# Kernel tuning notes

Measured on AMD Instinct MI355X. Metric: run time of the kernel, lower is better.

The kernel has to match this reference:

```python
import jax, jax.numpy as jnp
import numpy as np

N = 20000   # nodes
E = 160000  # edges
C = 512     # input_size / channels
D = 16      # edge_size
H = 256     # hidden_size
EPS = 1e-5  # BatchNorm eps (eval mode, init running stats: mean=0, var=1)


def setup_inputs() -> dict:
    key = jax.random.key(0)
    ks = jax.random.split(key, 24)
    w = lambda k, shape: (jax.random.normal(k, shape, jnp.float32) * 0.02)
    inp = {
        "x": jax.random.normal(ks[0], (N, C), jnp.float32),
        "edge_index": jax.random.randint(ks[1], (2, E), 0, N, jnp.int32),
        "edge_attr": jax.random.normal(ks[2], (E, D), jnp.float32),
        "goal_feat": jax.random.normal(ks[3], (N, C), jnp.float32),
        # CGConv 1
        "Wf1": w(ks[4], (2 * C + D, C)), "bf1": jnp.zeros((C,), jnp.float32),
        "Ws1": w(ks[5], (2 * C + D, C)), "bs1": jnp.zeros((C,), jnp.float32),
        "g1": jnp.ones((C,), jnp.float32), "be1": jnp.zeros((C,), jnp.float32),
        # CGConv 2
        "Wf2": w(ks[6], (2 * C + D, C)), "bf2": jnp.zeros((C,), jnp.float32),
        "Ws2": w(ks[7], (2 * C + D, C)), "bs2": jnp.zeros((C,), jnp.float32),
        "g2": jnp.ones((C,), jnp.float32), "be2": jnp.zeros((C,), jnp.float32),
        # GCNConv 3, 4
        "W3": w(ks[8], (C, H)), "b3": jnp.zeros((H,), jnp.float32),
        "W4": w(ks[9], (H, H)), "b4": jnp.zeros((H,), jnp.float32),
        # distance MLP: Lin(H+C -> C), ReLU, Lin(C -> 1)
        "Wd1": w(ks[10], (H + C, C)), "bd1": jnp.zeros((C,), jnp.float32),
        "Wd2": w(ks[11], (C, 1)), "bd2": jnp.zeros((1,), jnp.float32),
    }
    return inp


def cg_conv(x, src, dst, edge_attr, Wf, bf, Ws, bs, gamma, beta):
    # PyG CGConv: z = x_i || x_j || e;  m = sigmoid(lin_f(z)) * softplus(lin_s(z))
    # aggr='add' at targets, BatchNorm (eval, init stats), residual.
    z = jnp.concatenate([x[dst], x[src], edge_attr], axis=-1)  # [E, 2C+D]
    m = jax.nn.sigmoid(z @ Wf + bf) * jax.nn.softplus(z @ Ws + bs)  # [E, C]
    agg = jax.ops.segment_sum(m, dst, num_segments=N)  # [N, C]
    agg = agg * (gamma / jnp.sqrt(1.0 + EPS)) + beta   # BN eval (mean=0, var=1)
    return agg + x


def gcn_conv(x, src, dst, W, b):
    # PyG GCNConv with add_self_loops=True, normalize=True
    h = x @ W  # [N, out]
    loop = jnp.arange(N, dtype=src.dtype)
    s = jnp.concatenate([src, loop])
    d = jnp.concatenate([dst, loop])
    deg = jax.ops.segment_sum(jnp.ones_like(d, jnp.float32), d, num_segments=N)
    dinv = jnp.where(deg > 0, jax.lax.rsqrt(jnp.maximum(deg, 1.0)), 0.0)
    norm = dinv[s] * dinv[d]  # [E+N]
    out = jax.ops.segment_sum(norm[:, None] * h[s], d, num_segments=N)
    return out + b


def reference(x, edge_index, edge_attr, goal_feat,
              Wf1, bf1, Ws1, bs1, g1, be1,
              Wf2, bf2, Ws2, bs2, g2, be2,
              W3, b3, W4, b4, Wd1, bd1, Wd2, bd2):
    src = edge_index[0]  # x_j (source)
    dst = edge_index[1]  # x_i (target)
    h = jax.nn.relu(cg_conv(x, src, dst, edge_attr, Wf1, bf1, Ws1, bs1, g1, be1))
    h = jax.nn.relu(cg_conv(h, src, dst, edge_attr, Wf2, bf2, Ws2, bs2, g2, be2))
    h = jax.nn.relu(gcn_conv(h, src, dst, W3, b3))
    h = jax.nn.relu(gcn_conv(h, src, dst, W4, b4))
    z = jnp.concatenate([h, goal_feat], axis=1)  # [N, H+C]
    pred_dist = jax.nn.relu(z @ Wd1 + bd1) @ Wd2 + bd2  # [N, 1]
    return pred_dist, h
```

## Files before the change

### kernel.cpp

```cpp
#include <hip/hip_runtime.h>
#include <stdint.h>

#define NNODES 20000
#define NEDGES 160000
#define NPAD   20096

typedef float f32x4 __attribute__((ext_vector_type(4)));
typedef float f32x2 __attribute__((ext_vector_type(2)));
typedef short s16x8 __attribute__((ext_vector_type(8)));

__device__ __forceinline__ float b2f(unsigned short b) {
    unsigned int u = ((unsigned int)b) << 16;
    return __builtin_bit_cast(float, u);
}
__device__ __forceinline__ unsigned short f2b(float f) {
    unsigned int u = __builtin_bit_cast(unsigned int, f);
    unsigned int r = (u + 0x7FFFu + ((u >> 16) & 1u)) >> 16;
    return (unsigned short)r;
}
__device__ __forceinline__ f32x2 unpack2(unsigned int u) {
    f32x2 r;
    r.x = __builtin_bit_cast(float, u << 16);
    r.y = __builtin_bit_cast(float, u & 0xFFFF0000u);
    return r;
}

__global__ __launch_bounds__(256) void gemm_bt_kernel(
    const unsigned short* __restrict__ A,
    const unsigned short* __restrict__ BT,
    float* __restrict__ Cf,
    unsigned short* __restrict__ Cb,
    int M, int N, int K,
    const float* __restrict__ bias)
{
    __shared__ unsigned short As[128 * 32];
    __shared__ unsigned short Bs[128 * 32];
    const int tid  = threadIdx.x;
    const int wid  = tid >> 6;
    const int lane = tid & 63;
    const int bm = blockIdx.x * 128;
    const int bn = blockIdx.y * 128;
    const int wm = (wid & 1) * 64;
    const int wn = (wid >> 1) * 64;

    f32x4 acc[4][4];
#pragma unroll
    for (int i = 0; i < 4; i++)
#pragma unroll
        for (int j = 0; j < 4; j++) acc[i][j] = {0.f, 0.f, 0.f, 0.f};

    for (int k0 = 0; k0 < K; k0 += 32) {
#pragma unroll
        for (int r = 0; r < 2; r++) {
            int flat = r * 256 + tid;
            int row  = flat >> 2;
            int part = flat & 3;
            const unsigned short* ga = A  + (size_t)(bm + row) * K + k0 + part * 8;
            const unsigned short* gb = BT + (size_t)(bn + row) * K + k0 + part * 8;
            __builtin_amdgcn_global_load_lds(
                (const __attribute__((address_space(1))) unsigned int*)ga,
                (__attribute__((address_space(3))) unsigned int*)&As[flat * 8], 16, 0, 0);
            __builtin_amdgcn_global_load_lds(
                (const __attribute__((address_space(1))) unsigned int*)gb,
                (__attribute__((address_space(3))) unsigned int*)&Bs[flat * 8], 16, 0, 0);
        }
        __syncthreads();

        const int kq = (lane >> 4) * 8;
        const int rl = lane & 15;
        s16x8 af[4], bfr[4];
#pragma unroll
        for (int mi = 0; mi < 4; mi++)
            af[mi] = *(const s16x8*)&As[(wm + mi * 16 + rl) * 32 + kq];
#pragma unroll
        for (int ni = 0; ni < 4; ni++)
            bfr[ni] = *(const s16x8*)&Bs[(wn + ni * 16 + rl) * 32 + kq];
#pragma unroll
        for (int mi = 0; mi < 4; mi++)
#pragma unroll
            for (int ni = 0; ni < 4; ni++)
                acc[mi][ni] = __builtin_amdgcn_mfma_f32_16x16x32_bf16(
                    af[mi], bfr[ni], acc[mi][ni], 0, 0, 0);
        __syncthreads();
    }

    const int cl = lane & 15;
    const int rq = (lane >> 4) * 4;
#pragma unroll
    for (int mi = 0; mi < 4; mi++)
#pragma unroll
        for (int ni = 0; ni < 4; ni++)
#pragma unroll
            for (int r = 0; r < 4; r++) {
                int row = bm + wm + mi * 16 + rq + r;
                int col = bn + wn + ni * 16 + cl;
                float v = acc[mi][ni][r];
                if (Cb) {
                    if (bias) v = fmaxf(v + bias[col], 0.f);
                    Cb[(size_t)row * N + col] = f2b(v);
                } else {
                    Cf[(size_t)row * N + col] = v;
                }
            }
}

__global__ void count_kernel(const int* __restrict__ ei, int* __restrict__ counts) {
    int e = blockIdx.x * blockDim.x + threadIdx.x;
    if (e < NEDGES) atomicAdd(&counts[ei[NEDGES + e]], 1);
}

__global__ __launch_bounds__(1024) void scan_kernel(const int* __restrict__ counts,
                                                    int* __restrict__ row_ptr)
{
    __shared__ int sdata[1024];
    const int t = threadIdx.x;
    int vals[20];
    const int base = t * 20;
    int lsum = 0;
#pragma unroll
    for (int j = 0; j < 20; j++) {
        int idx = base + j;
        int v = (idx < NNODES) ? counts[idx] : 0;
        vals[j] = v; lsum += v;
    }
    sdata[t] = lsum;
    __syncthreads();
    for (int off = 1; off < 1024; off <<= 1) {
        int v = (t >= off) ? sdata[t - off] : 0;
        __syncthreads();
        sdata[t] += v;
        __syncthreads();
    }
    int run = sdata[t] - lsum;
#pragma unroll
    for (int j = 0; j < 20; j++) {
        int idx = base + j;
        if (idx < NNODES) row_ptr[idx] = run;
        run += vals[j];
    }
    if (t == 1023) row_ptr[NNODES] = sdata[1023];
}

__global__ void fill_kernel(const int* __restrict__ ei,
                            const int* __restrict__ row_ptr,
                            int* __restrict__ cursor,
                            int2* __restrict__ csr)
{
    int e = blockIdx.x * blockDim.x + threadIdx.x;
    if (e >= NEDGES) return;
    int dst = ei[NEDGES + e];
    int p = row_ptr[dst] + atomicAdd(&cursor[dst], 1);
    csr[p] = make_int2(ei[e], e);
}

__global__ void dinv_kernel(const int* __restrict__ row_ptr, float* __restrict__ dinv) {
    int i = blockIdx.x * blockDim.x + threadIdx.x;
    if (i < NNODES) {
        int deg = row_ptr[i + 1] - row_ptr[i] + 1;
        dinv[i] = rsqrtf((float)deg);
    }
}

__global__ void pad_copy_kernel(const float* __restrict__ src,
                                unsigned short* __restrict__ dst,
                                int valid_rows, int cols, long total)
{
    long idx = (long)blockIdx.x * blockDim.x + threadIdx.x;
    if (idx >= total) return;
    int n = (int)(idx / cols);
    dst[idx] = (n < valid_rows) ? f2b(src[idx]) : (unsigned short)0;
}

__global__ void pack_cgw_kernel(const float* __restrict__ Wf,
                                const float* __restrict__ Ws,
                                unsigned short* __restrict__ out)
{
    int idx = blockIdx.x * blockDim.x + threadIdx.x;
    if (idx >= 2048 * 512) return;
    int j = idx >> 9;
    int k = idx & 511;
    float v;
    if (j < 512)       v = Wf[(size_t)k * 512 + j];
    else if (j < 1024) v = Wf[(size_t)(512 + k) * 512 + (j - 512)];
    else if (j < 1536) v = Ws[(size_t)k * 512 + (j - 1024)];
    else               v = Ws[(size_t)(512 + k) * 512 + (j - 1536)];
    out[idx] = f2b(v);
}

__global__ void pack_t_kernel(const float* __restrict__ W,
                              unsigned short* __restrict__ WT,
                              int K, int Nout)
{
    long idx = (long)blockIdx.x * blockDim.x + threadIdx.x;
    if (idx >= (long)K * Nout) return;
    int j = (int)(idx / K);
    int k = (int)(idx % K);
    WT[idx] = f2b(W[(size_t)k * Nout + j]);
}

__global__ __launch_bounds__(256, 1) void cg_gather_kernel(
    const unsigned short* __restrict__ P,
    const int* __restrict__ row_ptr,
    const int2* __restrict__ csr,
    const float* __restrict__ ea,
    const float* __restrict__ Wf,
    const float* __restrict__ Ws,
    const float* __restrict__ bfv,
    const float* __restrict__ bsv,
    const float* __restrict__ g,
    const float* __restrict__ be,
    const float* __restrict__ xresf,
    const unsigned short* __restrict__ xresb,
    unsigned short* __restrict__ hout)
{
    const int n   = blockIdx.x;
    const int tid = threadIdx.x;
    const int c0  = tid * 2;
    if (n >= NNODES) {
        *(unsigned int*)&hout[(size_t)n * 512 + c0] = 0;
        return;
    }
    f32x2 wf[16], wsv[16];
#pragma unroll
    for (int k = 0; k < 16; k++) {
        const size_t rb = (size_t)(1024 + k) * 512;
        wf[k]  = *(const f32x2*)&Wf[rb + c0];
        wsv[k] = *(const f32x2*)&Ws[rb + c0];
    }
    const unsigned short* Pd = P + (size_t)n * 2048;
    const f32x2 baseF = unpack2(*(const unsigned int*)(Pd + c0))        + *(const f32x2*)&bfv[c0];
    const f32x2 baseS = unpack2(*(const unsigned int*)(Pd + 1024 + c0)) + *(const f32x2*)&bsv[c0];

    f32x2 acc = {0.f, 0.f};
    const int i0 = row_ptr[n], i1 = row_ptr[n + 1];

    if (i0 < i1) {
        int2 se = csr[i0];
        {
            const float4* ep = (const float4*)(ea + (size_t)se.y * 16);
            const unsigned short* Ps = P + (size_t)se.x * 2048;
            float4 e0 = ep[0], e1 = ep[1], e2 = ep[2], e3 = ep[3];
            unsigned int pf = *(const unsigned int*)(Ps + 512 + c0);
            unsigned int ps = *(const unsigned int*)(Ps + 1536 + c0);

            for (int i = i0; i < i1; i++) {
                float4 c0v = e0, c1v = e1, c2v = e2, c3v = e3;
                unsigned int cpf = pf, cps = ps;
                if (i + 1 < i1) {
                    int2 se2 = csr[i + 1];
                    const float4* ep2 = (const float4*)(ea + (size_t)se2.y * 16);
                    const unsigned short* Ps2 = P + (size_t)se2.x * 2048;
                    e0 = ep2[0]; e1 = ep2[1]; e2 = ep2[2]; e3 = ep2[3];
                    pf = *(const unsigned int*)(Ps2 + 512 + c0);
                    ps = *(const unsigned int*)(Ps2 + 1536 + c0);
                }
                f32x2 f = baseF + unpack2(cpf);
                f32x2 s = baseS + unpack2(cps);
                const float ek[16] = {c0v.x, c0v.y, c0v.z, c0v.w,
                                      c1v.x, c1v.y, c1v.z, c1v.w,
                                      c2v.x, c2v.y, c2v.z, c2v.w,
                                      c3v.x, c3v.y, c3v.z, c3v.w};
#pragma unroll
                for (int k = 0; k < 16; k++) {
                    f32x2 ev = {ek[k], ek[k]};
                    f = __builtin_elementwise_fma(ev, wf[k], f);
                    s = __builtin_elementwise_fma(ev, wsv[k], s);
                }
                float sp0 = __logf(1.f + __expf(s.x));
                float sp1 = __logf(1.f + __expf(s.y));
                float sg0 = __builtin_amdgcn_rcpf(1.f + __expf(-f.x));
                float sg1 = __builtin_amdgcn_rcpf(1.f + __expf(-f.y));
                acc.x = fmaf(sp0, sg0, acc.x);
                acc.y = fmaf(sp1, sg1, acc.y);
            }
        }
    }
    const float rs = rsqrtf(1.f + 1e-5f);
    f32x2 res;
    if (xresf) {
        res = *(const f32x2*)&xresf[(size_t)n * 512 + c0];
    } else {
        res = unpack2(*(const unsigned int*)&xresb[(size_t)n * 512 + c0]);
    }
    const f32x2 gv  = *(const f32x2*)&g[c0];
    const f32x2 bev = *(const f32x2*)&be[c0];
    float v0 = fmaxf(acc.x * (gv.x * rs) + bev.x + res.x, 0.f);
    float v1 = fmaxf(acc.y * (gv.y * rs) + bev.y + res.y, 0.f);
    unsigned int packed = (unsigned int)f2b(v0) | ((unsigned int)f2b(v1) << 16);
    *(unsigned int*)&hout[(size_t)n * 512 + c0] = packed;
}

__global__ __launch_bounds__(256) void gcn_gather_kernel(
    const unsigned short* __restrict__ pre,
    const int* __restrict__ row_ptr,
    const int2* __restrict__ csr,
    const float* __restrict__ dinv,
    const float* __restrict__ b,
    unsigned short* __restrict__ hout,
    float* __restrict__ doutf)
{
    const int n = blockIdx.x;
    const int c = threadIdx.x;
    if (n >= NNODES) {
        hout[(size_t)n * 256 + c] = 0;
        return;
    }
    const float din = dinv[n];
    float acc = 0.f;
    const int i0 = row_ptr[n], i1 = row_ptr[n + 1];
    for (int i = i0; i < i1; i++) {
        const int src = csr[i].x;
        acc = fmaf(dinv[src], b2f(pre[(size_t)src * 256 + c]), acc);
    }
    float self = b2f(pre[(size_t)n * 256 + c]);
    float v = fmaxf(acc * din + din * din * self + b[c], 0.f);
    hout[(size_t)n * 256 + c] = f2b(v);
    if (doutf) doutf[(size_t)n * 256 + c] = v;
}

__global__ void build_zc_kernel(const unsigned short* __restrict__ h4,
                                const float* __restrict__ goal,
                                unsigned short* __restrict__ zc)
{
    long idx = (long)blockIdx.x * blockDim.x + threadIdx.x;
    if (idx >= (long)NPAD * 768) return;
    int n = (int)(idx / 768);
    int c = (int)(idx % 768);
    unsigned short v = 0;
    if (n < NNODES)
        v = (c < 256) ? h4[(size_t)n * 256 + c]
                      : f2b(goal[(size_t)n * 512 + (c - 256)]);
    zc[idx] = v;
}

__global__ __launch_bounds__(256) void final_dot_kernel(
    const unsigned short* __restrict__ t,
    const float* __restrict__ Wd2,
    const float* __restrict__ bd2,
    float* __restrict__ pred)
{
    const int lane = threadIdx.x & 63;
    const int wid  = threadIdx.x >> 6;
    float w[8];
#pragma unroll
    for (int i = 0; i < 8; i++) w[i] = Wd2[lane * 8 + i];
    const float bd = bd2[0];
    for (int n = blockIdx.x * 4 + wid; n < NNODES; n += gridDim.x * 4) {
        const unsigned short* tp = t + (size_t)n * 512 + lane * 8;
        float s = 0.f;
#pragma unroll
        for (int i = 0; i < 8; i++) s = fmaf(b2f(tp[i]), w[i], s);
#pragma unroll
        for (int off = 32; off; off >>= 1) s += __shfl_xor(s, off, 64);
        if (lane == 0) pred[n] = s + bd;
    }
}

extern "C" void kernel_launch(void* const* d_in, const int* in_sizes, int n_in,
                              void* d_out, int out_size, void* d_ws, size_t ws_size,
                              hipStream_t stream)
{
    (void)in_sizes; (void)n_in; (void)out_size; (void)ws_size;
    const float* x    = (const float*)d_in[0];
    const int*   ei   = (const int*)d_in[1];
    const float* ea   = (const float*)d_in[2];
    const float* goal = (const float*)d_in[3];
    const float* Wf1  = (const float*)d_in[4];
    const float* bf1  = (const float*)d_in[5];
    const float* Ws1  = (const float*)d_in[6];
    const float* bs1  = (const float*)d_in[7];
    const float* g1   = (const float*)d_in[8];
    const float* be1  = (const float*)d_in[9];
    const float* Wf2  = (const float*)d_in[10];
    const float* bf2  = (const float*)d_in[11];
    const float* Ws2  = (const float*)d_in[12];
    const float* bs2  = (const float*)d_in[13];
    const float* g2   = (const float*)d_in[14];
    const float* be2  = (const float*)d_in[15];
    const float* W3   = (const float*)d_in[16];
    const float* b3   = (const float*)d_in[17];
    const float* W4   = (const float*)d_in[18];
    const float* b4   = (const float*)d_in[19];
    const float* Wd1  = (const float*)d_in[20];
    const float* bd1  = (const float*)d_in[21];
    const float* Wd2  = (const float*)d_in[22];
    const float* bd2  = (const float*)d_in[23];
    float* outp = (float*)d_out;

    char* ws = (char*)d_ws;
    size_t off = 0;
    auto alloc = [&](size_t bytes) -> char* {
        char* p = ws + off;
        off += (bytes + 255) & ~(size_t)255;
        return p;
    };
    unsigned short* P     = (unsigned short*)alloc((size_t)NPAD * 2048 * 2);
    unsigned short* bufA  = (unsigned short*)alloc((size_t)NPAD * 512 * 2);
    unsigned short* bufB  = (unsigned short*)alloc((size_t)NPAD * 512 * 2);
    unsigned short* bufC  = (unsigned short*)alloc((size_t)NPAD * 512 * 2);
    unsigned short* wpack = (unsigned short*)alloc((size_t)2048 * 512 * 2);
    int*            counts  = (int*)alloc((size_t)NNODES * 4);
    int*            row_ptr = (int*)alloc((size_t)(NNODES + 1) * 4);
    int2*           csr     = (int2*)alloc((size_t)NEDGES * 8);
    float*          dinv    = (float*)alloc((size_t)NNODES * 4);

    unsigned short* xpad  = bufA;
    unsigned short* h1    = bufB;
    unsigned short* h2    = bufA;
    unsigned short* pre_b = bufB;
    unsigned short* h3    = bufC;
    unsigned short* h4    = bufA;
    unsigned short* zc    = P;
    unsigned short* tb    = P + (size_t)NPAD * 1024;

    const int B = 256;

    hipMemsetAsync(counts, 0, (size_t)NNODES * 4, stream);
    count_kernel<<<(NEDGES + B - 1) / B, B, 0, stream>>>(ei, counts);
    scan_kernel<<<1, 1024, 0, stream>>>(counts, row_ptr);
    hipMemsetAsync(counts, 0, (size_t)NNODES * 4, stream);
    fill_kernel<<<(NEDGES + B - 1) / B, B, 0, stream>>>(ei, row_ptr, counts, csr);
    dinv_kernel<<<(NNODES + B - 1) / B, B, 0, stream>>>(row_ptr, dinv);

    {
        long tot = (long)NPAD * 512;
        pad_copy_kernel<<<(unsigned)((tot + B - 1) / B), B, 0, stream>>>(x, xpad, NNODES, 512, tot);
    }

    dim3 gBig(NPAD / 128, 2048 / 128);

    pack_cgw_kernel<<<(2048 * 512 + B - 1) / B, B, 0, stream>>>(Wf1, Ws1, wpack);
    gemm_bt_kernel<<<gBig, B, 0, stream>>>(xpad, wpack, nullptr, P, NPAD, 2048, 512, nullptr);
    cg_gather_kernel<<<NPAD, B, 0, stream>>>(P, row_ptr, csr, ea,
                                             Wf1, Ws1, bf1, bs1, g1, be1,
                                             x, nullptr, h1);

    pack_cgw_kernel<<<(2048 * 512 + B - 1) / B, B, 0, stream>>>(Wf2, Ws2, wpack);
    gemm_bt_kernel<<<gBig, B, 0, stream>>>(h1, wpack, nullptr, P, NPAD, 2048, 512, nullptr);
    cg_gather_kernel<<<NPAD, B, 0, stream>>>(P, row_ptr, csr, ea,
                                             Wf2, Ws2, bf2, bs2, g2, be2,
                                             nullptr, h1, h2);

    pack_t_kernel<<<(256 * 512 + B - 1) / B, B, 0, stream>>>(W3, wpack, 512, 256);
    gemm_bt_kernel<<<dim3(NPAD / 128, 2), B, 0, stream>>>(h2, wpack, nullptr, pre_b, NPAD, 256, 512, nullptr);
    gcn_gather_kernel<<<NPAD, B, 0, stream>>>(pre_b, row_ptr, csr, dinv, b3, h3, (float*)nullptr);

    pack_t_kernel<<<(256 * 256 + B - 1) / B, B, 0, stream>>>(W4, wpack, 256, 256);
    gemm_bt_kernel<<<dim3(NPAD / 128, 2), B, 0, stream>>>(h3, wpack, nullptr, pre_b, NPAD, 256, 256, nullptr);
    gcn_gather_kernel<<<NPAD, B, 0, stream>>>(pre_b, row_ptr, csr, dinv, b4, h4, outp + NNODES);

    build_zc_kernel<<<(unsigned)(((long)NPAD * 768 + B - 1) / B), B, 0, stream>>>(h4, goal, zc);
    pack_t_kernel<<<(512 * 768 + B - 1) / B, B, 0, stream>>>(Wd1, wpack, 768, 512);
    gemm_bt_kernel<<<dim3(NPAD / 128, 4), B, 0, stream>>>(zc, wpack, nullptr, tb, NPAD, 512, 768, bd1);
    final_dot_kernel<<<512, B, 0, stream>>>(tb, Wd2, bd2, outp);
}
```

Baseline: 865.2 us.

## Interleave CGConv projection columns and batch nodes per block in gather kernels

The packed CGConv weight is reordered so that, for each channel pair, the dst-f, dst-s values and the src-f, src-s values sit next to each other. The gather can then fetch both with one 8-byte load per side instead of two scattered 4-byte loads. The CG gather processes four nodes per block, amortizing the per-block loads of the 16 edge-weight rows and the per-channel constants. Neighbor indices are made wave-uniform via readfirstlane. The GCN gather handles two nodes per block with two channels per thread, using packed loads and software prefetch of the next neighbor; the trade-off is fewer blocks and more serial work per block in the CG gather.

```diff
diff --git a/kernel.cpp b/kernel.cpp
--- a/kernel.cpp
+++ b/kernel.cpp
@@ -179,11 +179,12 @@
     if (idx >= 2048 * 512) return;
     int j = idx >> 9;
     int k = idx & 511;
-    float v;
-    if (j < 512)       v = Wf[(size_t)k * 512 + j];
-    else if (j < 1024) v = Wf[(size_t)(512 + k) * 512 + (j - 512)];
-    else if (j < 1536) v = Ws[(size_t)k * 512 + (j - 1024)];
-    else               v = Ws[(size_t)(512 + k) * 512 + (j - 1536)];
+    int half = (j >= 1024);
+    int jj = j & 1023;
+    int c  = (jj >> 2) * 2 + (jj & 1);
+    int fs = (jj >> 1) & 1;
+    const float* W = fs ? Ws : Wf;
+    float v = W[(size_t)(half ? 512 + k : k) * 512 + c];
     out[idx] = f2b(v);
 }
 
@@ -198,6 +199,7 @@
     WT[idx] = f2b(W[(size_t)k * Nout + j]);
 }
 
+#define CG_NPB 4
 __global__ __launch_bounds__(256, 1) void cg_gather_kernel(
     const unsigned short* __restrict__ P,
     const int* __restrict__ row_ptr,
@@ -213,13 +215,10 @@
     const unsigned short* __restrict__ xresb,
     unsigned short* __restrict__ hout)
 {
-    const int n   = blockIdx.x;
     const int tid = threadIdx.x;
     const int c0  = tid * 2;
-    if (n >= NNODES) {
-        *(unsigned int*)&hout[(size_t)n * 512 + c0] = 0;
-        return;
-    }
+    const int nbase = blockIdx.x * CG_NPB;
+
     f32x2 wf[16], wsv[16];
 #pragma unroll
     for (int k = 0; k < 16; k++) {
@@ -227,35 +226,46 @@
         wf[k]  = *(const f32x2*)&Wf[rb + c0];
         wsv[k] = *(const f32x2*)&Ws[rb + c0];
     }
-    const unsigned short* Pd = P + (size_t)n * 2048;
-    const f32x2 baseF = unpack2(*(const unsigned int*)(Pd + c0))        + *(const f32x2*)&bfv[c0];
-    const f32x2 baseS = unpack2(*(const unsigned int*)(Pd + 1024 + c0)) + *(const f32x2*)&bsv[c0];
-
-    f32x2 acc = {0.f, 0.f};
-    const int i0 = row_ptr[n], i1 = row_ptr[n + 1];
-
-    if (i0 < i1) {
-        int2 se = csr[i0];
-        {
-            const float4* ep = (const float4*)(ea + (size_t)se.y * 16);
-            const unsigned short* Ps = P + (size_t)se.x * 2048;
+    const f32x2 bfx = *(const f32x2*)&bfv[c0];
+    const f32x2 bsx = *(const f32x2*)&bsv[c0];
+    const f32x2 gv  = *(const f32x2*)&g[c0];
+    const f32x2 bev = *(const f32x2*)&be[c0];
+    const float rs = rsqrtf(1.f + 1e-5f);
+
+    for (int n = nbase; n < nbase + CG_NPB; n++) {
+        if (n >= NNODES) {
+            *(unsigned int*)&hout[(size_t)n * 512 + c0] = 0;
+            continue;
+        }
+        const unsigned short* Pd = P + (size_t)n * 2048;
+        const uint2 qb = *(const uint2*)(Pd + c0 * 2);
+        const f32x2 baseF = unpack2(qb.x) + bfx;
+        const f32x2 baseS = unpack2(qb.y) + bsx;
+
+        f32x2 acc = {0.f, 0.f};
+        const int i0 = row_ptr[n], i1 = row_ptr[n + 1];
+
+        if (i0 < i1) {
+            int2 se = csr[i0];
+            int sx = __builtin_amdgcn_readfirstlane(se.x);
+            int sy = __builtin_amdgcn_readfirstlane(se.y);
+            const float4* ep = (const float4*)(ea + (size_t)sy * 16);
             float4 e0 = ep[0], e1 = ep[1], e2 = ep[2], e3 = ep[3];
-            unsigned int pf = *(const unsigned int*)(Ps + 512 + c0);
-            unsigned int ps = *(const unsigned int*)(Ps + 1536 + c0);
+            uint2 q = *(const uint2*)(P + (size_t)sx * 2048 + 1024 + c0 * 2);
 
             for (int i = i0; i < i1; i++) {
                 float4 c0v = e0, c1v = e1, c2v = e2, c3v = e3;
-                unsigned int cpf = pf, cps = ps;
+                uint2  cq  = q;
                 if (i + 1 < i1) {
                     int2 se2 = csr[i + 1];
-                    const float4* ep2 = (const float4*)(ea + (size_t)se2.y * 16);
-                    const unsigned short* Ps2 = P + (size_t)se2.x * 2048;
+                    int sx2 = __builtin_amdgcn_readfirstlane(se2.x);
+                    int sy2 = __builtin_amdgcn_readfirstlane(se2.y);
+                    const float4* ep2 = (const float4*)(ea + (size_t)sy2 * 16);
                     e0 = ep2[0]; e1 = ep2[1]; e2 = ep2[2]; e3 = ep2[3];
-                    pf = *(const unsigned int*)(Ps2 + 512 + c0);
-                    ps = *(const unsigned int*)(Ps2 + 1536 + c0);
+                    q = *(const uint2*)(P + (size_t)sx2 * 2048 + 1024 + c0 * 2);
                 }
-                f32x2 f = baseF + unpack2(cpf);
-                f32x2 s = baseS + unpack2(cps);
+                f32x2 f = baseF + unpack2(cq.x);
+                f32x2 s = baseS + unpack2(cq.y);
                 const float ek[16] = {c0v.x, c0v.y, c0v.z, c0v.w,
                                       c1v.x, c1v.y, c1v.z, c1v.w,
                                       c2v.x, c2v.y, c2v.z, c2v.w,
@@ -274,20 +284,17 @@
                 acc.y = fmaf(sp1, sg1, acc.y);
             }
         }
-    }
-    const float rs = rsqrtf(1.f + 1e-5f);
-    f32x2 res;
-    if (xresf) {
-        res = *(const f32x2*)&xresf[(size_t)n * 512 + c0];
-    } else {
-        res = unpack2(*(const unsigned int*)&xresb[(size_t)n * 512 + c0]);
-    }
-    const f32x2 gv  = *(const f32x2*)&g[c0];
-    const f32x2 bev = *(const f32x2*)&be[c0];
-    float v0 = fmaxf(acc.x * (gv.x * rs) + bev.x + res.x, 0.f);
-    float v1 = fmaxf(acc.y * (gv.y * rs) + bev.y + res.y, 0.f);
-    unsigned int packed = (unsigned int)f2b(v0) | ((unsigned int)f2b(v1) << 16);
-    *(unsigned int*)&hout[(size_t)n * 512 + c0] = packed;
+        f32x2 res;
+        if (xresf) {
+            res = *(const f32x2*)&xresf[(size_t)n * 512 + c0];
+        } else {
+            res = unpack2(*(const unsigned int*)&xresb[(size_t)n * 512 + c0]);
+        }
+        float v0 = fmaxf(acc.x * (gv.x * rs) + bev.x + res.x, 0.f);
+        float v1 = fmaxf(acc.y * (gv.y * rs) + bev.y + res.y, 0.f);
+        unsigned int packed = (unsigned int)f2b(v0) | ((unsigned int)f2b(v1) << 16);
+        *(unsigned int*)&hout[(size_t)n * 512 + c0] = packed;
+    }
 }
 
 __global__ __launch_bounds__(256) void gcn_gather_kernel(
@@ -299,23 +306,42 @@
     unsigned short* __restrict__ hout,
     float* __restrict__ doutf)
 {
-    const int n = blockIdx.x;
-    const int c = threadIdx.x;
+    const int tid = threadIdx.x;
+    const int n = blockIdx.x * 2 + (tid >> 7);
+    const int c = (tid & 127) * 2;
     if (n >= NNODES) {
-        hout[(size_t)n * 256 + c] = 0;
+        if (n < NPAD) *(unsigned int*)&hout[(size_t)n * 256 + c] = 0;
         return;
     }
     const float din = dinv[n];
-    float acc = 0.f;
+    f32x2 acc = {0.f, 0.f};
     const int i0 = row_ptr[n], i1 = row_ptr[n + 1];
-    for (int i = i0; i < i1; i++) {
-        const int src = csr[i].x;
-        acc = fmaf(dinv[src], b2f(pre[(size_t)src * 256 + c]), acc);
-    }
-    float self = b2f(pre[(size_t)n * 256 + c]);
-    float v = fmaxf(acc * din + din * din * self + b[c], 0.f);
-    hout[(size_t)n * 256 + c] = f2b(v);
-    if (doutf) doutf[(size_t)n * 256 + c] = v;
+    if (i0 < i1) {
+        int sx = __builtin_amdgcn_readfirstlane(csr[i0].x);
+        float dv = dinv[sx];
+        unsigned int pv = *(const unsigned int*)&pre[(size_t)sx * 256 + c];
+        for (int i = i0; i < i1; i++) {
+            float cdv = dv; unsigned int cpv = pv;
+            if (i + 1 < i1) {
+                int sx2 = __builtin_amdgcn_readfirstlane(csr[i + 1].x);
+                dv = dinv[sx2];
+                pv = *(const unsigned int*)&pre[(size_t)sx2 * 256 + c];
+            }
+            f32x2 p = unpack2(cpv);
+            acc.x = fmaf(cdv, p.x, acc.x);
+            acc.y = fmaf(cdv, p.y, acc.y);
+        }
+    }
+    f32x2 self = unpack2(*(const unsigned int*)&pre[(size_t)n * 256 + c]);
+    const f32x2 bv = *(const f32x2*)&b[c];
+    float v0 = fmaxf(fmaf(acc.x, din, din * din * self.x) + bv.x, 0.f);
+    float v1 = fmaxf(fmaf(acc.y, din, din * din * self.y) + bv.y, 0.f);
+    *(unsigned int*)&hout[(size_t)n * 256 + c] =
+        (unsigned int)f2b(v0) | ((unsigned int)f2b(v1) << 16);
+    if (doutf) {
+        f32x2 vv = {v0, v1};
+        *(f32x2*)&doutf[(size_t)n * 256 + c] = vv;
+    }
 }
 
 __global__ void build_zc_kernel(const unsigned short* __restrict__ h4,
@@ -431,23 +457,23 @@
 
     pack_cgw_kernel<<<(2048 * 512 + B - 1) / B, B, 0, stream>>>(Wf1, Ws1, wpack);
     gemm_bt_kernel<<<gBig, B, 0, stream>>>(xpad, wpack, nullptr, P, NPAD, 2048, 512, nullptr);
-    cg_gather_kernel<<<NPAD, B, 0, stream>>>(P, row_ptr, csr, ea,
-                                             Wf1, Ws1, bf1, bs1, g1, be1,
-                                             x, nullptr, h1);
+    cg_gather_kernel<<<NPAD / CG_NPB, B, 0, stream>>>(P, row_ptr, csr, ea,
+                                                      Wf1, Ws1, bf1, bs1, g1, be1,
+                                                      x, nullptr, h1);
 
     pack_cgw_kernel<<<(2048 * 512 + B - 1) / B, B, 0, stream>>>(Wf2, Ws2, wpack);
     gemm_bt_kernel<<<gBig, B, 0, stream>>>(h1, wpack, nullptr, P, NPAD, 2048, 512, nullptr);
-    cg_gather_kernel<<<NPAD, B, 0, stream>>>(P, row_ptr, csr, ea,
-                                             Wf2, Ws2, bf2, bs2, g2, be2,
-                                             nullptr, h1, h2);
+    cg_gather_kernel<<<NPAD / CG_NPB, B, 0, stream>>>(P, row_ptr, csr, ea,
+                                                      Wf2, Ws2, bf2, bs2, g2, be2,
+                                                      nullptr, h1, h2);
 
     pack_t_kernel<<<(256 * 512 + B - 1) / B, B, 0, stream>>>(W3, wpack, 512, 256);
     gemm_bt_kernel<<<dim3(NPAD / 128, 2), B, 0, stream>>>(h2, wpack, nullptr, pre_b, NPAD, 256, 512, nullptr);
-    gcn_gather_kernel<<<NPAD, B, 0, stream>>>(pre_b, row_ptr, csr, dinv, b3, h3, (float*)nullptr);
+    gcn_gather_kernel<<<NPAD / 2, B, 0, stream>>>(pre_b, row_ptr, csr, dinv, b3, h3, (float*)nullptr);
 
     pack_t_kernel<<<(256 * 256 + B - 1) / B, B, 0, stream>>>(W4, wpack, 256, 256);
     gemm_bt_kernel<<<dim3(NPAD / 128, 2), B, 0, stream>>>(h3, wpack, nullptr, pre_b, NPAD, 256, 256, nullptr);
-    gcn_gather_kernel<<<NPAD, B, 0, stream>>>(pre_b, row_ptr, csr, dinv, b4, h4, outp + NNODES);
+    gcn_gather_kernel<<<NPAD / 2, B, 0, stream>>>(pre_b, row_ptr, csr, dinv, b4, h4, outp + NNODES);
 
     build_zc_kernel<<<(unsigned)(((long)NPAD * 768 + B - 1) / B), B, 0, stream>>>(h4, goal, zc);
     pack_t_kernel<<<(512 * 768 + B - 1) / B, B, 0, stream>>>(Wd1, wpack, 768, 512);
```

Result: faster. 825.8 us (-4.5%).
